# Kernel optimization log

Measured on AMD Instinct MI355X. Metric: run time of the kernel, lower is better.

Reference implementation:

```python
import jax, jax.numpy as jnp
import numpy as np

N, D_IN, D_HID, D_OUT, ORDER = 8192, 512, 1024, 64, 3

def setup_inputs() -> dict:
    key = jax.random.key(0)
    k = jax.random.split(key, 5)
    x = jax.random.normal(k[0], (N, D_IN), dtype=jnp.float32)
    adj = jax.random.uniform(k[1], (ORDER, N, N), dtype=jnp.float32)
    W1 = jax.random.normal(k[2], (ORDER, D_IN, D_HID), dtype=jnp.float32) * (1.0 / np.sqrt(D_IN))
    b1 = jnp.zeros((D_HID,), dtype=jnp.float32)
    W2 = jax.random.normal(k[3], (ORDER, D_HID, D_OUT), dtype=jnp.float32) * (1.0 / np.sqrt(D_HID))
    b2 = jnp.zeros((D_OUT,), dtype=jnp.float32)
    return {"x": x, "preprocessed": adj, "W1": W1, "b1": b1, "W2": W2, "b2": b2}

def multi_val_gc(x, adj, W, b):
    # x: [N, in], adj: [order, N, N], W: [order, in, out]
    xw = jnp.einsum('ni,kio->kno', x, W)          # [order, N, out]
    out = jnp.einsum('knm,kmo->no', adj, xw)      # sum over orders
    return out + b

def reference(x, preprocessed, W1, b1, W2, b2):
    h = multi_val_gc(x, preprocessed, W1, b1)
    h = jax.nn.relu(h)
    # dropout is identity in eval mode
    h = multi_val_gc(h, preprocessed, W2, b2)
    return jax.nn.log_softmax(h, axis=1)
```

## Files before the change

### kernel.cpp

```cpp
#include <hip/hip_runtime.h>
#include <hip/hip_bf16.h>
#include <cstdint>
#include <cstddef>


typedef __bf16 bf16_t;
typedef __bf16 bf16x8 __attribute__((ext_vector_type(8)));
typedef __bf16 bf16x4 __attribute__((ext_vector_type(4)));
typedef float  f32x4  __attribute__((ext_vector_type(4)));

#define NROWS 8192
#define DIN   512
#define DHID  1024
#define DOUT  64
#define ORD   3
#define KTOT  24576

#define GLDS(g, l) __builtin_amdgcn_global_load_lds( \
    (__attribute__((address_space(1))) void*)(g),    \
    (__attribute__((address_space(3))) void*)(l), 16, 0, 0)


__global__ void k_cvt_x(const float* __restrict__ x, bf16_t* __restrict__ xb) {
  int i = blockIdx.x * blockDim.x + threadIdx.x;
  const float4* p = reinterpret_cast<const float4*>(x) + (size_t)i * 2;
  float4 v0 = p[0], v1 = p[1];
  bf16x8 o;
  o[0]=(bf16_t)v0.x; o[1]=(bf16_t)v0.y; o[2]=(bf16_t)v0.z; o[3]=(bf16_t)v0.w;
  o[4]=(bf16_t)v1.x; o[5]=(bf16_t)v1.y; o[6]=(bf16_t)v1.z; o[7]=(bf16_t)v1.w;
  *reinterpret_cast<bf16x8*>(xb + (size_t)i * 8) = o;
}

__global__ void k_cvt_adj(const float* __restrict__ a, bf16_t* __restrict__ ab) {
  size_t i = (size_t)blockIdx.x * blockDim.x + threadIdx.x;
  const size_t stride = (size_t)gridDim.x * blockDim.x;
  const float4* src = reinterpret_cast<const float4*>(a);
#pragma unroll 4
  for (int it = 0; it < 48; ++it, i += stride) {
    float4 v0 = src[i * 2], v1 = src[i * 2 + 1];
    bf16x8 o;
    o[0]=(bf16_t)v0.x; o[1]=(bf16_t)v0.y; o[2]=(bf16_t)v0.z; o[3]=(bf16_t)v0.w;
    o[4]=(bf16_t)v1.x; o[5]=(bf16_t)v1.y; o[6]=(bf16_t)v1.z; o[7]=(bf16_t)v1.w;
    *reinterpret_cast<bf16x8*>(ab + i * 8) = o;
  }
}

__global__ void k_transpose_cvt(const float* __restrict__ src, bf16_t* __restrict__ dst,
                                int R, int C) {
  __shared__ float tile[64][65];
  int ord = blockIdx.z;
  src += (size_t)ord * R * C;
  dst += (size_t)ord * R * C;
  int c0 = blockIdx.x * 64, r0 = blockIdx.y * 64;
  for (int i = 0; i < 16; ++i) {
    int idx = i * 256 + threadIdx.x;
    int r = idx >> 6, c = idx & 63;
    tile[r][c] = src[(size_t)(r0 + r) * C + c0 + c];
  }
  __syncthreads();
  for (int i = 0; i < 16; ++i) {
    int idx = i * 256 + threadIdx.x;
    int cc = idx >> 6, rr = idx & 63;
    dst[(size_t)(c0 + cc) * R + r0 + rr] = (bf16_t)tile[rr][cc];
  }
}

__global__ __launch_bounds__(256) void k_gemm_xw1(
    const bf16_t* __restrict__ xb,
    const bf16_t* __restrict__ w1t,
    bf16_t* __restrict__ xw1t)
{
  __shared__ bf16_t As[128 * 64];
  __shared__ bf16_t Bs[128 * 64];
  int ntile = blockIdx.x, mtile = blockIdx.y, ord = blockIdx.z;
  int tid = threadIdx.x, lane = tid & 63, wid = tid >> 6;
  int wm = wid >> 1, wn = wid & 1;
  int sl = (lane & 7) ^ (lane >> 3);
  f32x4 acc[4][4] = {};
  const bf16_t* w1o = w1t + (size_t)ord * DHID * DIN;
  for (int kt = 0; kt < DIN; kt += 64) {
    for (int j = 0; j < 4; ++j) {
      int q = wid * 4 + j;
      int row = q * 8 + (lane >> 3);
      GLDS(xb + (size_t)(mtile * 128 + row) * DIN + kt + sl * 8, &As[q * 512]);
    }
    for (int j = 0; j < 4; ++j) {
      int q = wid * 4 + j;
      int row = q * 8 + (lane >> 3);
      GLDS(w1o + (size_t)(ntile * 128 + row) * DIN + kt + sl * 8, &Bs[q * 512]);
    }
    __syncthreads();
    for (int ks = 0; ks < 2; ++ks) {
      int psl = ((ks << 2) + (lane >> 4)) ^ (lane & 7);
      bf16x8 a[4], b[4];
      for (int f = 0; f < 4; ++f)
        a[f] = *reinterpret_cast<const bf16x8*>(&As[(wm * 64 + f * 16 + (lane & 15)) * 64 + psl * 8]);
      for (int f = 0; f < 4; ++f)
        b[f] = *reinterpret_cast<const bf16x8*>(&Bs[(wn * 64 + f * 16 + (lane & 15)) * 64 + psl * 8]);
      for (int fm = 0; fm < 4; ++fm)
        for (int fn = 0; fn < 4; ++fn)
          acc[fm][fn] = __builtin_amdgcn_mfma_f32_16x16x32_bf16(a[fm], b[fn], acc[fm][fn], 0, 0, 0);
    }
    __syncthreads();
  }
  for (int fm = 0; fm < 4; ++fm)
    for (int fn = 0; fn < 4; ++fn) {
      int o  = ntile * 128 + wn * 64 + fn * 16 + (lane & 15);
      int n0 = mtile * 128 + wm * 64 + fm * 16 + ((lane >> 4) << 2);
      bf16x4 v;
      v[0] = (bf16_t)acc[fm][fn][0]; v[1] = (bf16_t)acc[fm][fn][1];
      v[2] = (bf16_t)acc[fm][fn][2]; v[3] = (bf16_t)acc[fm][fn][3];
      *reinterpret_cast<bf16x4*>(&xw1t[(size_t)o * KTOT + ord * NROWS + n0]) = v;
    }
}

__global__ __launch_bounds__(256) void k_gemm_h(
    const bf16_t* __restrict__ adjb,
    const bf16_t* __restrict__ xw1t,
    const float* __restrict__ b1,
    bf16_t* __restrict__ h)
{
  __shared__ bf16_t As[2][128 * 64];
  __shared__ bf16_t Bs[2][128 * 64];
  int d = blockIdx.x;
  int x = d & 7;
  int s = d >> 3;
  int j = s >> 3;
  int w = s & 7;
  int mtile = (2 * j + (x & 1)) * 4 + (w >> 1);
  int ntile = ((x >> 1) & 3) * 2 + (w & 1);
  int tid = threadIdx.x, lane = tid & 63, wid = tid >> 6;
  int wm = wid >> 1, wn = wid & 1;
  int sl = (lane & 7) ^ (lane >> 3);
  const size_t NN = (size_t)NROWS * NROWS;
  f32x4 acc[4][4] = {};
  const int NT = KTOT / 64;

  auto stage = [&](int buf, int kt) {
    int kk = kt * 64;
    int ord = kk >> 13, mcol = kk & 8191;
    const bf16_t* ao = adjb + (size_t)ord * NN + (size_t)(mtile * 128) * NROWS + mcol;
#pragma unroll
    for (int jj = 0; jj < 4; ++jj) {
      int q = wid * 4 + jj;
      int row = q * 8 + (lane >> 3);
      GLDS(ao + (size_t)row * NROWS + sl * 8, &As[buf][q * 512]);
    }
#pragma unroll
    for (int jj = 0; jj < 4; ++jj) {
      int q = wid * 4 + jj;
      int row = q * 8 + (lane >> 3);
      GLDS(xw1t + (size_t)(ntile * 128 + row) * KTOT + kk + sl * 8, &Bs[buf][q * 512]);
    }
  };

  auto compute = [&](int cur) {
    const bf16_t* Ac = &As[cur][0];
    const bf16_t* Bc = &Bs[cur][0];
#pragma unroll
    for (int ks = 0; ks < 2; ++ks) {
      int psl = ((ks << 2) + (lane >> 4)) ^ (lane & 7);
      bf16x8 a[4], b[4];
      for (int f = 0; f < 4; ++f)
        a[f] = *reinterpret_cast<const bf16x8*>(&Ac[(wm * 64 + f * 16 + (lane & 15)) * 64 + psl * 8]);
      for (int f = 0; f < 4; ++f)
        b[f] = *reinterpret_cast<const bf16x8*>(&Bc[(wn * 64 + f * 16 + (lane & 15)) * 64 + psl * 8]);
      for (int fm = 0; fm < 4; ++fm)
        for (int fn = 0; fn < 4; ++fn)
          acc[fm][fn] = __builtin_amdgcn_mfma_f32_16x16x32_bf16(a[fm], b[fn], acc[fm][fn], 0, 0, 0);
    }
  };

  stage(0, 0);
  for (int t = 0; t < NT - 1; ++t) {
    int cur = t & 1;
    stage(cur ^ 1, t + 1);
    asm volatile("s_waitcnt vmcnt(8)" ::: "memory");
    __builtin_amdgcn_s_barrier();
    compute(cur);
    asm volatile("" ::: "memory");
    __builtin_amdgcn_s_barrier();
  }
  asm volatile("s_waitcnt vmcnt(0)" ::: "memory");
  __builtin_amdgcn_s_barrier();
  compute((NT - 1) & 1);

  for (int fm = 0; fm < 4; ++fm)
    for (int fn = 0; fn < 4; ++fn) {
      int o  = ntile * 128 + wn * 64 + fn * 16 + (lane & 15);
      float bias = b1[o];
      int n0 = mtile * 128 + wm * 64 + fm * 16 + ((lane >> 4) << 2);
      for (int jj = 0; jj < 4; ++jj) {
        float v = acc[fm][fn][jj] + bias;
        v = v > 0.0f ? v : 0.0f;
        h[(size_t)(n0 + jj) * DHID + o] = (bf16_t)v;
      }
    }
}

__global__ __launch_bounds__(256) void k_gemm_xw2(
    const bf16_t* __restrict__ h,
    const bf16_t* __restrict__ w2t,
    bf16_t* __restrict__ xw2t)
{
  __shared__ bf16_t As[128 * 64];
  __shared__ bf16_t Bs[64 * 64];
  int mtile = blockIdx.x, ord = blockIdx.y;
  int tid = threadIdx.x, lane = tid & 63, wid = tid >> 6;
  int wm = wid >> 1, wn = wid & 1;
  int sl = (lane & 7) ^ (lane >> 3);
  f32x4 acc[4][2] = {};
  const bf16_t* w2o = w2t + (size_t)ord * DOUT * DHID;
  for (int kt = 0; kt < DHID; kt += 64) {
    for (int j = 0; j < 4; ++j) {
      int q = wid * 4 + j;
      int row = q * 8 + (lane >> 3);
      GLDS(h + (size_t)(mtile * 128 + row) * DHID + kt + sl * 8, &As[q * 512]);
    }
    for (int j = 0; j < 2; ++j) {
      int q = wid * 2 + j;
      int row = q * 8 + (lane >> 3);
      GLDS(w2o + (size_t)row * DHID + kt + sl * 8, &Bs[q * 512]);
    }
    __syncthreads();
    for (int ks = 0; ks < 2; ++ks) {
      int psl = ((ks << 2) + (lane >> 4)) ^ (lane & 7);
      bf16x8 a[4], b[2];
      for (int f = 0; f < 4; ++f)
        a[f] = *reinterpret_cast<const bf16x8*>(&As[(wm * 64 + f * 16 + (lane & 15)) * 64 + psl * 8]);
      for (int f = 0; f < 2; ++f)
        b[f] = *reinterpret_cast<const bf16x8*>(&Bs[(wn * 32 + f * 16 + (lane & 15)) * 64 + psl * 8]);
      for (int fm = 0; fm < 4; ++fm)
        for (int fn = 0; fn < 2; ++fn)
          acc[fm][fn] = __builtin_amdgcn_mfma_f32_16x16x32_bf16(a[fm], b[fn], acc[fm][fn], 0, 0, 0);
    }
    __syncthreads();
  }
  for (int fm = 0; fm < 4; ++fm)
    for (int fn = 0; fn < 2; ++fn) {
      int o2 = wn * 32 + fn * 16 + (lane & 15);
      int n0 = mtile * 128 + wm * 64 + fm * 16 + ((lane >> 4) << 2);
      bf16x4 v;
      v[0] = (bf16_t)acc[fm][fn][0]; v[1] = (bf16_t)acc[fm][fn][1];
      v[2] = (bf16_t)acc[fm][fn][2]; v[3] = (bf16_t)acc[fm][fn][3];
      *reinterpret_cast<bf16x4*>(&xw2t[(size_t)o2 * KTOT + ord * NROWS + n0]) = v;
    }
}

__global__ __launch_bounds__(256) void k_gemm_out(
    const bf16_t* __restrict__ adjb,
    const bf16_t* __restrict__ xw2t,
    float* __restrict__ part)
{
  __shared__ bf16_t As[128 * 64];
  __shared__ bf16_t Bs[64 * 64];
  int mtile = blockIdx.x, ksp = blockIdx.y;
  int tid = threadIdx.x, lane = tid & 63, wid = tid >> 6;
  int wm = wid >> 1, wn = wid & 1;
  int sl = (lane & 7) ^ (lane >> 3);
  const size_t NN = (size_t)NROWS * NROWS;
  f32x4 acc[4][2] = {};
  for (int kt = ksp * 24; kt < ksp * 24 + 24; ++kt) {
    int kk = kt * 64;
    int ord = kk >> 13, mcol = kk & 8191;
    const bf16_t* ao = adjb + (size_t)ord * NN + (size_t)(mtile * 128) * NROWS + mcol;
    for (int j = 0; j < 4; ++j) {
      int q = wid * 4 + j;
      int row = q * 8 + (lane >> 3);
      GLDS(ao + (size_t)row * NROWS + sl * 8, &As[q * 512]);
    }
    for (int j = 0; j < 2; ++j) {
      int q = wid * 2 + j;
      int row = q * 8 + (lane >> 3);
      GLDS(xw2t + (size_t)row * KTOT + kk + sl * 8, &Bs[q * 512]);
    }
    __syncthreads();
    for (int ks = 0; ks < 2; ++ks) {
      int psl = ((ks << 2) + (lane >> 4)) ^ (lane & 7);
      bf16x8 a[4], b[2];
      for (int f = 0; f < 4; ++f)
        a[f] = *reinterpret_cast<const bf16x8*>(&As[(wm * 64 + f * 16 + (lane & 15)) * 64 + psl * 8]);
      for (int f = 0; f < 2; ++f)
        b[f] = *reinterpret_cast<const bf16x8*>(&Bs[(wn * 32 + f * 16 + (lane & 15)) * 64 + psl * 8]);
      for (int fm = 0; fm < 4; ++fm)
        for (int fn = 0; fn < 2; ++fn)
          acc[fm][fn] = __builtin_amdgcn_mfma_f32_16x16x32_bf16(a[fm], b[fn], acc[fm][fn], 0, 0, 0);
    }
    __syncthreads();
  }
  float* pout = part + (size_t)ksp * NROWS * DOUT;
  for (int fm = 0; fm < 4; ++fm)
    for (int fn = 0; fn < 2; ++fn) {
      int o2 = wn * 32 + fn * 16 + (lane & 15);
      int n0 = mtile * 128 + wm * 64 + fm * 16 + ((lane >> 4) << 2);
      for (int j = 0; j < 4; ++j)
        pout[(size_t)(n0 + j) * DOUT + o2] = acc[fm][fn][j];
    }
}

__global__ void k_logsoftmax(const float* __restrict__ part, const float* __restrict__ b2,
                             float* __restrict__ out) {
  int wid = threadIdx.x >> 6, lane = threadIdx.x & 63;
  int n = blockIdx.x * 4 + wid;
  size_t s = (size_t)NROWS * DOUT;
  float v = b2[lane];
#pragma unroll
  for (int p = 0; p < 16; ++p)
    v += part[(size_t)p * s + (size_t)n * DOUT + lane];
  float mx = v;
  for (int d = 32; d; d >>= 1) mx = fmaxf(mx, __shfl_xor(mx, d));
  float e = expf(v - mx);
  float sum = e;
  for (int d = 32; d; d >>= 1) sum += __shfl_xor(sum, d);
  out[(size_t)n * DOUT + lane] = (v - mx) - logf(sum);
}

__global__ __launch_bounds__(256) void k_gemm_h_f32(
    const float* __restrict__ adj, const bf16_t* __restrict__ xw1t,
    const float* __restrict__ b1, bf16_t* __restrict__ h)
{
  __shared__ bf16_t As[128 * 64];
  __shared__ bf16_t Bs[128 * 64];
  int d = blockIdx.x;
  int xcd = d & 7, idx = d >> 3;
  int mtile = xcd * 8 + (idx >> 3), ntile = idx & 7;
  int tid = threadIdx.x, lane = tid & 63, wid = tid >> 6;
  int wm = wid >> 1, wn = wid & 1;
  int sl = (lane & 7) ^ (lane >> 3);
  f32x4 acc[4][4] = {};
  for (int kt = 0; kt < KTOT / 64; ++kt) {
    int kk0 = kt * 64;
    int ord = kk0 >> 13, mcol = kk0 & 8191;
    for (int j = 0; j < 4; ++j) {
      int q = wid * 4 + j;
      int row = q * 8 + (lane >> 3);
      GLDS(xw1t + (size_t)(ntile * 128 + row) * KTOT + kk0 + sl * 8, &Bs[q * 512]);
    }
    const float* abase = adj + (size_t)ord * NROWS * NROWS + (size_t)(mtile * 128) * NROWS + mcol;
    bf16x8 st[4]; int mrow[4], kb[4];
    for (int i = 0; i < 4; ++i) {
      int c = i * 256 + tid;
      mrow[i] = c >> 3; kb[i] = c & 7;
      const float4* p = reinterpret_cast<const float4*>(abase + (size_t)mrow[i] * NROWS + kb[i] * 8);
      float4 v0 = p[0], v1 = p[1];
      bf16x8 o;
      o[0]=(bf16_t)v0.x; o[1]=(bf16_t)v0.y; o[2]=(bf16_t)v0.z; o[3]=(bf16_t)v0.w;
      o[4]=(bf16_t)v1.x; o[5]=(bf16_t)v1.y; o[6]=(bf16_t)v1.z; o[7]=(bf16_t)v1.w;
      st[i] = o;
    }
    for (int i = 0; i < 4; ++i)
      *reinterpret_cast<bf16x8*>(&As[mrow[i] * 64 + (kb[i] ^ (mrow[i] & 7)) * 8]) = st[i];
    __syncthreads();
    for (int ks = 0; ks < 2; ++ks) {
      int psl = ((ks << 2) + (lane >> 4)) ^ (lane & 7);
      bf16x8 a[4], b[4];
      for (int f = 0; f < 4; ++f)
        a[f] = *reinterpret_cast<const bf16x8*>(&As[(wm * 64 + f * 16 + (lane & 15)) * 64 + psl * 8]);
      for (int f = 0; f < 4; ++f)
        b[f] = *reinterpret_cast<const bf16x8*>(&Bs[(wn * 64 + f * 16 + (lane & 15)) * 64 + psl * 8]);
      for (int fm = 0; fm < 4; ++fm)
        for (int fn = 0; fn < 4; ++fn)
          acc[fm][fn] = __builtin_amdgcn_mfma_f32_16x16x32_bf16(a[fm], b[fn], acc[fm][fn], 0, 0, 0);
    }
    __syncthreads();
  }
  for (int fm = 0; fm < 4; ++fm)
    for (int fn = 0; fn < 4; ++fn) {
      int o  = ntile * 128 + wn * 64 + fn * 16 + (lane & 15);
      float bias = b1[o];
      int n0 = mtile * 128 + wm * 64 + fm * 16 + ((lane >> 4) << 2);
      for (int j = 0; j < 4; ++j) {
        float v = acc[fm][fn][j] + bias;
        v = v > 0.0f ? v : 0.0f;
        h[(size_t)(n0 + j) * DHID + o] = (bf16_t)v;
      }
    }
}

__global__ __launch_bounds__(256) void k_gemm_out_f32(
    const float* __restrict__ adj, const bf16_t* __restrict__ xw2t,
    float* __restrict__ part)
{
  __shared__ bf16_t As[128 * 64];
  __shared__ bf16_t Bs[64 * 64];
  int mtile = blockIdx.x, ksp = blockIdx.y;
  int tid = threadIdx.x, lane = tid & 63, wid = tid >> 6;
  int wm = wid >> 1, wn = wid & 1;
  int sl = (lane & 7) ^ (lane >> 3);
  f32x4 acc[4][2] = {};
  for (int kt = ksp * 24; kt < ksp * 24 + 24; ++kt) {
    int kk0 = kt * 64;
    int ord = kk0 >> 13, mcol = kk0 & 8191;
    for (int j = 0; j < 2; ++j) {
      int q = wid * 2 + j;
      int row = q * 8 + (lane >> 3);
      GLDS(xw2t + (size_t)row * KTOT + kk0 + sl * 8, &Bs[q * 512]);
    }
    const float* abase = adj + (size_t)ord * NROWS * NROWS + (size_t)(mtile * 128) * NROWS + mcol;
    bf16x8 st[4]; int mrow[4], kb[4];
    for (int i = 0; i < 4; ++i) {
      int c = i * 256 + tid;
      mrow[i] = c >> 3; kb[i] = c & 7;
      const float4* p = reinterpret_cast<const float4*>(abase + (size_t)mrow[i] * NROWS + kb[i] * 8);
      float4 v0 = p[0], v1 = p[1];
      bf16x8 o;
      o[0]=(bf16_t)v0.x; o[1]=(bf16_t)v0.y; o[2]=(bf16_t)v0.z; o[3]=(bf16_t)v0.w;
      o[4]=(bf16_t)v1.x; o[5]=(bf16_t)v1.y; o[6]=(bf16_t)v1.z; o[7]=(bf16_t)v1.w;
      st[i] = o;
    }
    for (int i = 0; i < 4; ++i)
      *reinterpret_cast<bf16x8*>(&As[mrow[i] * 64 + (kb[i] ^ (mrow[i] & 7)) * 8]) = st[i];
    __syncthreads();
    for (int ks = 0; ks < 2; ++ks) {
      int psl = ((ks << 2) + (lane >> 4)) ^ (lane & 7);
      bf16x8 a[4], b[2];
      for (int f = 0; f < 4; ++f)
        a[f] = *reinterpret_cast<const bf16x8*>(&As[(wm * 64 + f * 16 + (lane & 15)) * 64 + psl * 8]);
      for (int f = 0; f < 2; ++f)
        b[f] = *reinterpret_cast<const bf16x8*>(&Bs[(wn * 32 + f * 16 + (lane & 15)) * 64 + psl * 8]);
      for (int fm = 0; fm < 4; ++fm)
        for (int fn = 0; fn < 2; ++fn)
          acc[fm][fn] = __builtin_amdgcn_mfma_f32_16x16x32_bf16(a[fm], b[fn], acc[fm][fn], 0, 0, 0);
    }
    __syncthreads();
  }
  float* pout = part + (size_t)ksp * NROWS * DOUT;
  for (int fm = 0; fm < 4; ++fm)
    for (int fn = 0; fn < 2; ++fn) {
      int o2 = wn * 32 + fn * 16 + (lane & 15);
      int n0 = mtile * 128 + wm * 64 + fm * 16 + ((lane >> 4) << 2);
      for (int j = 0; j < 4; ++j)
        pout[(size_t)(n0 + j) * DOUT + o2] = acc[fm][fn][j];
    }
}

extern "C" void kernel_launch(void* const* d_in, const int* in_sizes, int n_in,
                              void* d_out, int out_size, void* d_ws, size_t ws_size,
                              hipStream_t stream) {
  const float* x   = (const float*)d_in[0];
  const float* adj = (const float*)d_in[1];
  const float* W1  = (const float*)d_in[2];
  const float* b1  = (const float*)d_in[3];
  const float* W2  = (const float*)d_in[4];
  const float* b2  = (const float*)d_in[5];
  float* out = (float*)d_out;
  char* ws = (char*)d_ws;

  const size_t ADJB_SZ = 402653184ULL;
  const size_t NEED    = 484835328ULL;

  if (ws_size >= NEED) {
    bf16_t* adjb = (bf16_t*)(ws + 0);
    bf16_t* xb   = (bf16_t*)(ws + ADJB_SZ);
    bf16_t* w1t  = (bf16_t*)(ws + ADJB_SZ + 8388608);
    bf16_t* w2t  = (bf16_t*)(ws + ADJB_SZ + 11534336);
    bf16_t* xw1t = (bf16_t*)(ws + ADJB_SZ + 11927552);
    bf16_t* h    = (bf16_t*)(ws + ADJB_SZ + 62259200);
    bf16_t* xw2t = (bf16_t*)(ws + ADJB_SZ + 79036416);
    float*  part = (float*)(ws + ADJB_SZ + 11927552);

    k_cvt_adj<<<2048, 256, 0, stream>>>(adj, adjb);
    k_cvt_x<<<2048, 256, 0, stream>>>(x, xb);
    k_transpose_cvt<<<dim3(16, 8, 3), 256, 0, stream>>>(W1, w1t, DIN, DHID);
    k_transpose_cvt<<<dim3(1, 16, 3), 256, 0, stream>>>(W2, w2t, DHID, DOUT);
    k_gemm_xw1<<<dim3(8, 64, 3), 256, 0, stream>>>(xb, w1t, xw1t);
    k_gemm_h<<<512, 256, 0, stream>>>(adjb, xw1t, b1, h);
    k_gemm_xw2<<<dim3(64, 3), 256, 0, stream>>>(h, w2t, xw2t);
    k_gemm_out<<<dim3(64, 16), 256, 0, stream>>>(adjb, xw2t, part);
    k_logsoftmax<<<2048, 256, 0, stream>>>(part, b2, out);
  } else {
    bf16_t* xb   = (bf16_t*)(ws + 0);
    bf16_t* w1t  = (bf16_t*)(ws + 8388608);
    bf16_t* w2t  = (bf16_t*)(ws + 11534336);
    bf16_t* xw1t = (bf16_t*)(ws + 11927552);
    bf16_t* h    = (bf16_t*)(ws + 62259200);
    bf16_t* xw2t = (bf16_t*)(ws + 79036416);
    float*  part = (float*)(ws + 11927552);

    k_cvt_x<<<2048, 256, 0, stream>>>(x, xb);
    k_transpose_cvt<<<dim3(16, 8, 3), 256, 0, stream>>>(W1, w1t, DIN, DHID);
    k_transpose_cvt<<<dim3(1, 16, 3), 256, 0, stream>>>(W2, w2t, DHID, DOUT);
    k_gemm_xw1<<<dim3(8, 64, 3), 256, 0, stream>>>(xb, w1t, xw1t);
    k_gemm_h_f32<<<512, 256, 0, stream>>>(adj, xw1t, b1, h);
    k_gemm_xw2<<<dim3(64, 3), 256, 0, stream>>>(h, w2t, xw2t);
    k_gemm_out_f32<<<dim3(64, 16), 256, 0, stream>>>(adj, xw2t, part);
    k_logsoftmax<<<2048, 256, 0, stream>>>(part, b2, out);
  }
}
```

Before: 942.7 us.

## Use 256x256 split-K tiles for the adjacency GEMM with a separate reduce pass

Replaces the 128x128 double-buffered adjacency×XW1 GEMM with a 256x256-tile kernel of 512 threads that splits K in two, writes fp32 partial sums, and adds a separate reduce kernel that applies bias and ReLU. Larger tiles raise arithmetic intensity and cut redundant adj/xw1t reads from global memory. In exchange the new kernel has no double buffering (a single LDS buffer with two barriers per step), holds 128 fp32 accumulators per thread, and adds a 64MB partial-sum round trip. The fallback 128 kernel also gets a simpler XCD block mapping, and the path only runs when the workspace is large enough.

New measurement: 950.1 us. Within noise of the previous version (+0.8%).

```diff
diff --git a/kernel.cpp b/kernel.cpp
--- a/kernel.cpp
+++ b/kernel.cpp
@@ -114,21 +114,102 @@
     }
 }
 
-__global__ __launch_bounds__(256) void k_gemm_h(
+__global__ __launch_bounds__(512) void k_gemm_h256(
     const bf16_t* __restrict__ adjb,
     const bf16_t* __restrict__ xw1t,
-    const float* __restrict__ b1,
-    bf16_t* __restrict__ h)
+    float* __restrict__ hpart)
+{
+  __shared__ bf16_t As[256 * 64];
+  __shared__ bf16_t Bs[256 * 64];
+  int d = blockIdx.x;
+  int xcd = d & 7;
+  int s = d >> 3;
+  int ksp = xcd & 1;
+  int mtile = (xcd >> 1) * 8 + (s >> 2);
+  int ntile = s & 3;
+  int tid = threadIdx.x, lane = tid & 63, wid = tid >> 6;
+  int wm = wid >> 2, wn = wid & 3;
+  int sl = (lane & 7) ^ (lane >> 3);
+  const size_t NN = (size_t)NROWS * NROWS;
+  f32x4 acc[8][4] = {};
+  const int T0 = ksp * 192, NT = 192;
+
+  for (int t = 0; t < NT; ++t) {
+    int kk = (T0 + t) * 64;
+    int ord = kk >> 13, mcol = kk & 8191;
+    const bf16_t* ao = adjb + (size_t)ord * NN + (size_t)(mtile * 256) * NROWS + mcol;
+#pragma unroll
+    for (int j = 0; j < 4; ++j) {
+      int q = wid * 4 + j;
+      int row = q * 8 + (lane >> 3);
+      GLDS(ao + (size_t)row * NROWS + sl * 8, &As[q * 512]);
+    }
+#pragma unroll
+    for (int j = 0; j < 4; ++j) {
+      int q = wid * 4 + j;
+      int row = q * 8 + (lane >> 3);
+      GLDS(xw1t + (size_t)(ntile * 256 + row) * KTOT + kk + sl * 8, &Bs[q * 512]);
+    }
+    __syncthreads();
+#pragma unroll
+    for (int ks = 0; ks < 2; ++ks) {
+      int psl = ((ks << 2) + (lane >> 4)) ^ (lane & 7);
+      bf16x8 a[8], b[4];
+#pragma unroll
+      for (int f = 0; f < 8; ++f)
+        a[f] = *reinterpret_cast<const bf16x8*>(&As[(wm * 128 + f * 16 + (lane & 15)) * 64 + psl * 8]);
+#pragma unroll
+      for (int f = 0; f < 4; ++f)
+        b[f] = *reinterpret_cast<const bf16x8*>(&Bs[(wn * 64 + f * 16 + (lane & 15)) * 64 + psl * 8]);
+#pragma unroll
+      for (int fm = 0; fm < 8; ++fm)
+#pragma unroll
+        for (int fn = 0; fn < 4; ++fn)
+          acc[fm][fn] = __builtin_amdgcn_mfma_f32_16x16x32_bf16(a[fm], b[fn], acc[fm][fn], 0, 0, 0);
+    }
+    __syncthreads();
+  }
+
+  float* pout = hpart + (size_t)ksp * NROWS * DHID;
+#pragma unroll
+  for (int fm = 0; fm < 8; ++fm)
+#pragma unroll
+    for (int fn = 0; fn < 4; ++fn) {
+      int o  = ntile * 256 + wn * 64 + fn * 16 + (lane & 15);
+      int n0 = mtile * 256 + wm * 128 + fm * 16 + ((lane >> 4) << 2);
+      for (int j = 0; j < 4; ++j)
+        pout[(size_t)(n0 + j) * DHID + o] = acc[fm][fn][j];
+    }
+}
+
+__global__ void k_reduce_h(const float* __restrict__ hpart, const float* __restrict__ b1,
+                           bf16_t* __restrict__ h) {
+  size_t i4 = (size_t)blockIdx.x * blockDim.x + threadIdx.x;
+  size_t base = i4 * 4;
+  int col = (int)(base & (DHID - 1));
+  const size_t S = (size_t)NROWS * DHID;
+  float4 p0 = *reinterpret_cast<const float4*>(hpart + base);
+  float4 p1 = *reinterpret_cast<const float4*>(hpart + S + base);
+  float4 bb = *reinterpret_cast<const float4*>(b1 + col);
+  bf16x4 v;
+  float t0 = p0.x + p1.x + bb.x; v[0] = (bf16_t)(t0 > 0.f ? t0 : 0.f);
+  float t1 = p0.y + p1.y + bb.y; v[1] = (bf16_t)(t1 > 0.f ? t1 : 0.f);
+  float t2 = p0.z + p1.z + bb.z; v[2] = (bf16_t)(t2 > 0.f ? t2 : 0.f);
+  float t3 = p0.w + p1.w + bb.w; v[3] = (bf16_t)(t3 > 0.f ? t3 : 0.f);
+  *reinterpret_cast<bf16x4*>(h + base) = v;
+}
+
+__global__ __launch_bounds__(256) void k_gemm_h128(
+    const bf16_t* __restrict__ adjb, const bf16_t* __restrict__ xw1t,
+    const float* __restrict__ b1, bf16_t* __restrict__ h)
 {
   __shared__ bf16_t As[2][128 * 64];
   __shared__ bf16_t Bs[2][128 * 64];
   int d = blockIdx.x;
-  int x = d & 7;
-  int s = d >> 3;
-  int j = s >> 3;
-  int w = s & 7;
-  int mtile = (2 * j + (x & 1)) * 4 + (w >> 1);
-  int ntile = ((x >> 1) & 3) * 2 + (w & 1);
+  int xcd = d & 7;
+  int idx = d >> 3;
+  int mtile = xcd * 8 + (idx >> 3);
+  int ntile = idx & 7;
   int tid = threadIdx.x, lane = tid & 63, wid = tid >> 6;
   int wm = wid >> 1, wn = wid & 1;
   int sl = (lane & 7) ^ (lane >> 3);
@@ -153,7 +234,6 @@
       GLDS(xw1t + (size_t)(ntile * 128 + row) * KTOT + kk + sl * 8, &Bs[buf][q * 512]);
     }
   };
-
   auto compute = [&](int cur) {
     const bf16_t* Ac = &As[cur][0];
     const bf16_t* Bc = &Bs[cur][0];
@@ -446,10 +526,11 @@
   float* out = (float*)d_out;
   char* ws = (char*)d_ws;
 
-  const size_t ADJB_SZ = 402653184ULL;
-  const size_t NEED    = 484835328ULL;
-
-  if (ws_size >= NEED) {
+  const size_t ADJB_SZ  = 402653184ULL;
+  const size_t NEED_OLD = 484835328ULL;
+  const size_t NEED_NEW = 551944192ULL;
+
+  if (ws_size >= NEED_OLD) {
     bf16_t* adjb = (bf16_t*)(ws + 0);
     bf16_t* xb   = (bf16_t*)(ws + ADJB_SZ);
     bf16_t* w1t  = (bf16_t*)(ws + ADJB_SZ + 8388608);
@@ -457,14 +538,21 @@
     bf16_t* xw1t = (bf16_t*)(ws + ADJB_SZ + 11927552);
     bf16_t* h    = (bf16_t*)(ws + ADJB_SZ + 62259200);
     bf16_t* xw2t = (bf16_t*)(ws + ADJB_SZ + 79036416);
-    float*  part = (float*)(ws + ADJB_SZ + 11927552);
+    float*  hpart = (float*)(ws + ADJB_SZ + 82182144);
+    float*  part = (ws_size >= NEED_NEW) ? hpart
+                                         : (float*)(ws + ADJB_SZ + 11927552);
 
     k_cvt_adj<<<2048, 256, 0, stream>>>(adj, adjb);
     k_cvt_x<<<2048, 256, 0, stream>>>(x, xb);
     k_transpose_cvt<<<dim3(16, 8, 3), 256, 0, stream>>>(W1, w1t, DIN, DHID);
     k_transpose_cvt<<<dim3(1, 16, 3), 256, 0, stream>>>(W2, w2t, DHID, DOUT);
     k_gemm_xw1<<<dim3(8, 64, 3), 256, 0, stream>>>(xb, w1t, xw1t);
-    k_gemm_h<<<512, 256, 0, stream>>>(adjb, xw1t, b1, h);
+    if (ws_size >= NEED_NEW) {
+      k_gemm_h256<<<256, 512, 0, stream>>>(adjb, xw1t, hpart);
+      k_reduce_h<<<8192, 256, 0, stream>>>(hpart, b1, h);
+    } else {
+      k_gemm_h128<<<512, 256, 0, stream>>>(adjb, xw1t, b1, h);
+    }
     k_gemm_xw2<<<dim3(64, 3), 256, 0, stream>>>(h, w2t, xw2t);
     k_gemm_out<<<dim3(64, 16), 256, 0, stream>>>(adjb, xw2t, part);
     k_logsoftmax<<<2048, 256, 0, stream>>>(part, b2, out);
```
